# Performance work log

Hardware: AMD Instinct MI355X
Metric: run time of the kernel (lower is better)

Reference implementation:

```python
import jax, jax.numpy as jnp
import numpy as np

N, E, D, ED, H, MAXDEG = 50000, 800000, 128, 64, 8, 512
C = D // H


def _ln(x, g, b, eps=1e-5):
    m = jnp.mean(x, axis=-1, keepdims=True)
    v = jnp.var(x, axis=-1, keepdims=True)
    return (x - m) * jax.lax.rsqrt(v + eps) * g + b


def setup_inputs() -> dict:
    key = jax.random.key(0)
    ks = jax.random.split(key, 16)
    nrm = lambda k, s: jax.random.normal(k, s, jnp.float32) * 0.02
    return {
        "x": jax.random.normal(ks[0], (N, D), jnp.float32),
        "edge_index": jax.random.randint(ks[1], (2, E), 0, N, dtype=jnp.int32),
        "edge_attr": jax.random.normal(ks[2], (E, ED), jnp.float32),
        "deg_emb": nrm(ks[3], (MAXDEG, D)),
        "ln_g": jnp.ones((D,), jnp.float32), "ln_b": jnp.zeros((D,), jnp.float32),
        "Wq": nrm(ks[4], (D, D)), "bq": jnp.zeros((D,), jnp.float32),
        "Wk": nrm(ks[5], (D, D)), "bk": jnp.zeros((D,), jnp.float32),
        "Wv": nrm(ks[6], (D, D)), "bv": jnp.zeros((D,), jnp.float32),
        "We": nrm(ks[7], (ED, D)), "be": jnp.zeros((D,), jnp.float32),
        "Wskip": nrm(ks[8], (D, D)), "bskip": jnp.zeros((D,), jnp.float32),
        "W1": nrm(ks[9], (D, 4 * D)), "b1": jnp.zeros((4 * D,), jnp.float32),
        "W2": nrm(ks[10], (4 * D, D)), "b2": jnp.zeros((D,), jnp.float32),
        "eu_ln_g": jnp.ones((D,), jnp.float32), "eu_ln_b": jnp.zeros((D,), jnp.float32),
        "Wm": nrm(ks[11], (2 * D + ED, 2 * ED)), "bm": jnp.zeros((2 * ED,), jnp.float32),
        "eln_g": jnp.ones((ED,), jnp.float32), "eln_b": jnp.zeros((ED,), jnp.float32),
    }


def reference(x, edge_index, edge_attr, deg_emb, ln_g, ln_b, Wq, bq, Wk, bk, Wv, bv,
              We, be, Wskip, bskip, W1, b1, W2, b2, eu_ln_g, eu_ln_b, Wm, bm, eln_g, eln_b):
    n = x.shape[0]
    src, dst = edge_index[0], edge_index[1]

    # degree embedding: out-degree via scatter-add on src, clamped
    deg = jax.ops.segment_sum(jnp.ones_like(src), src, num_segments=n)
    x_in = x + deg_emb[jnp.clip(deg, 0, MAXDEG - 1)]

    # pre-norm (same LayerNorm module used for attn and ffn branches)
    h = _ln(x_in, ln_g, ln_b)

    # TransformerConv: per-edge gather -> score -> segment softmax -> scatter
    q = (h @ Wq + bq).reshape(n, H, C)
    k = (h @ Wk + bk).reshape(n, H, C)
    v = (h @ Wv + bv).reshape(n, H, C)
    e = (edge_attr @ We + be).reshape(-1, H, C)  # [E,H,C]

    ke = k[src] + e
    alpha = jnp.sum(q[dst] * ke, axis=-1) / jnp.sqrt(jnp.float32(C))  # [E,H]
    amax = jax.ops.segment_max(alpha, dst, num_segments=n)
    amax = jnp.where(jnp.isfinite(amax), amax, 0.0)
    ex = jnp.exp(alpha - amax[dst])
    denom = jax.ops.segment_sum(ex, dst, num_segments=n)
    w = ex / (denom[dst] + 1e-16)  # [E,H]

    msg = (v[src] + e) * w[:, :, None]
    out = jax.ops.segment_sum(msg, dst, num_segments=n).reshape(n, D)
    h_attn = out + h @ Wskip + bskip  # root skip on normed input

    x_attn = x_in + h_attn

    # FFN with pre-norm (norm_type == 'layer')
    hf = _ln(x_attn, ln_g, ln_b)
    ffn = jax.nn.gelu(hf @ W1 + b1, approximate=False) @ W2 + b2
    x_new = x_attn + ffn

    # EdgeUpdate: gated residual MLP on gathered node pairs
    xn = _ln(x_new, eu_ln_g, eu_ln_b)
    m = jnp.concatenate([xn[src], xn[dst], edge_attr], axis=-1)  # [E, 2D+ED]
    raw = jax.nn.relu(m @ Wm + bm)
    delta, gate = jnp.split(raw, 2, axis=-1)
    ea_new = _ln(edge_attr + jax.nn.sigmoid(gate) * delta, eln_g, eln_b)

    return x_new, ea_new
```

## Files before the change

### kernel.cpp

```cpp
#include <hip/hip_runtime.h>
#include <hip/hip_bf16.h>
#include <math.h>

constexpr int N_NODES = 50000;
constexpr int N_EDGES = 800000;
constexpr int D  = 128;
constexpr int ED = 64;

typedef __attribute__((ext_vector_type(8))) short short8;
typedef __attribute__((ext_vector_type(4))) float f32x4;

static __device__ __forceinline__ float allsum64(float v){
#pragma unroll
  for(int off=32; off>=1; off>>=1) v += __shfl_xor(v, off, 64);
  return v;
}

static __device__ __forceinline__ short bfs(float f){
  __hip_bfloat16 h = __float2bfloat16(f);
  return *reinterpret_cast<short*>(&h);
}
static __device__ __forceinline__ float bf2f(short s){
  __hip_bfloat16 h = *reinterpret_cast<__hip_bfloat16*>(&s);
  return __bfloat162float(h);
}
static __device__ __forceinline__ float lo16(int w){ return bf2f((short)(w & 0xffff)); }
static __device__ __forceinline__ float hi16(int w){ return bf2f((short)(((unsigned)w) >> 16)); }

template<typename T> __device__ __forceinline__ T cvt_out(float v);
template<> __device__ __forceinline__ float cvt_out<float>(float v){ return v; }
template<> __device__ __forceinline__ __hip_bfloat16 cvt_out<__hip_bfloat16>(float v){ return __float2bfloat16(v); }

__global__ void k_deg(const int* __restrict__ src, const int* __restrict__ dst,
                      int* __restrict__ deg, int* __restrict__ hist){
  int i = blockIdx.x*256 + threadIdx.x;
  if(i < N_EDGES){
    atomicAdd(&deg[src[i]], 1);
    atomicAdd(&hist[dst[i]], 1);
  }
}

__global__ __launch_bounds__(1024) void k_scan(const int* __restrict__ hist,
                                               int* __restrict__ rows,
                                               int* __restrict__ cursor){
  __shared__ int part[1024];
  const int t = threadIdx.x;
  const int CH = (N_NODES + 1023) / 1024;
  int base = t*CH;
  int s = 0;
  for(int i=0;i<CH;i++){ int idx=base+i; if(idx<N_NODES) s += hist[idx]; }
  part[t] = s; __syncthreads();
  for(int off=1; off<1024; off<<=1){
    int v = (t>=off) ? part[t-off] : 0;
    __syncthreads();
    part[t] += v;
    __syncthreads();
  }
  int run = part[t] - s;
  for(int i=0;i<CH;i++){
    int idx=base+i;
    if(idx<N_NODES){ rows[idx]=run; cursor[idx]=run; run += hist[idx]; }
  }
  if(t==1023) rows[N_NODES] = run;
}

__global__ void k_scatter(const int* __restrict__ src, const int* __restrict__ dst,
                          int* __restrict__ cursor,
                          int* __restrict__ perm, int* __restrict__ ssrc){
  int e = blockIdx.x*256 + threadIdx.x;
  if(e < N_EDGES){
    int p = atomicAdd(&cursor[dst[e]], 1);
    perm[p] = e;
    ssrc[p] = src[e];
  }
}

__global__ __launch_bounds__(256) void k_node_prep(
    const float* __restrict__ x, const int* __restrict__ deg,
    const float* __restrict__ deg_emb, const float* __restrict__ g,
    const float* __restrict__ b, float* __restrict__ xin, short* __restrict__ h){
  int node = blockIdx.x*4 + (threadIdx.x>>6);
  int lane = threadIdx.x & 63;
  if(node >= N_NODES) return;
  int dg = deg[node]; dg = dg > 511 ? 511 : dg;
  const float* xr = x + (size_t)node*D;
  const float* er = deg_emb + (size_t)dg*D;
  float a0 = xr[lane]    + er[lane];
  float a1 = xr[lane+64] + er[lane+64];
  float* xo = xin + (size_t)node*D;
  xo[lane] = a0; xo[lane+64] = a1;
  float s  = allsum64(a0+a1);
  float s2 = allsum64(a0*a0 + a1*a1);
  float mean = s * (1.f/128.f);
  float var  = s2 * (1.f/128.f) - mean*mean;
  float rs = rsqrtf(var + 1e-5f);
  h[(size_t)node*D + lane]    = bfs((a0-mean)*rs*g[lane]    + b[lane]);
  h[(size_t)node*D + lane+64] = bfs((a1-mean)*rs*g[lane+64] + b[lane+64]);
}

__global__ void k_pack(const float* __restrict__ Wq, const float* __restrict__ Wk,
                       const float* __restrict__ Wv, const float* __restrict__ Ws,
                       const float* __restrict__ bq, const float* __restrict__ bk,
                       const float* __restrict__ bv, const float* __restrict__ bs,
                       float* __restrict__ Wcat, float* __restrict__ bcat){
  int idx = blockIdx.x*256 + threadIdx.x;
  if(idx < D*4*D){
    int i = idx >> 9, j = idx & 511;
    int sel = j >> 7, jj = j & 127;
    const float* W = sel==0?Wq: sel==1?Wk: sel==2?Wv:Ws;
    Wcat[idx] = W[i*D + jj];
  } else if(idx < D*4*D + 4*D){
    int j = idx - D*4*D;
    int sel = j>>7, jj = j&127;
    const float* B = sel==0?bq: sel==1?bk: sel==2?bv:bs;
    bcat[j] = B[jj];
  }
}

__global__ void k_packWN(const float* __restrict__ W, short* __restrict__ out,
                         int K, int Nfull){
  int idx = blockIdx.x*256 + threadIdx.x;
  if(idx >= K*Nfull) return;
  int KC = K >> 5;
  int j  = idx & 7;
  int l  = (idx>>3) & 63;
  int cf = (idx>>9) & 7;
  int rest = idx >> 12;
  int kc = rest % KC;
  int nb = rest / KC;
  int k = kc*32 + ((l>>4)<<3) + j;
  int n = nb*128 + (cf<<4) + (l&15);
  out[idx] = bfs(W[(size_t)k*Nfull + n]);
}

__global__ void k_packWm12(const float* __restrict__ Wm, short* __restrict__ out){
  int idx = blockIdx.x*256 + threadIdx.x;
  if(idx >= 256*128) return;
  int j  = idx & 7;
  int l  = (idx>>3) & 63;
  int cf = (idx>>9) & 7;
  int rest = idx >> 12;
  int kc = rest & 3, nb = rest >> 2;
  int k = kc*32 + ((l>>4)<<3) + j;
  int n = (cf<<4) + (l&15);
  out[idx] = bfs(Wm[(size_t)(nb*128 + k)*128 + n]);
}

template<int ACT, int OMAP, typename OutT, typename AT>
__global__ __launch_bounds__(256) void k_gemm_mfma(
    const AT* __restrict__ A, const short* __restrict__ Wp,
    const float* __restrict__ bias,
    OutT* __restrict__ C, int M, int K, int Nfull){
  const int tid = threadIdx.x, lane = tid & 63, wid = tid >> 6;
  const int l16 = lane & 15, lg = lane >> 4;
  const int KC = K >> 5;
  const size_t rowb = (size_t)blockIdx.x*64 + wid*16;
  const int nb = blockIdx.y;
  size_t arow = rowb + l16; if(arow >= (size_t)M) arow = M-1;
  f32x4 acc[8] = {};
  const short8* Bg = ((const short8*)Wp) + (size_t)nb*KC*512 + lane;
  for(int kc=0; kc<KC; kc++){
    short8 a;
    if constexpr (sizeof(AT)==4){
      const float* ap = (const float*)A + arow*K + kc*32 + lg*8;
      float4 f0 = *(const float4*)ap;
      float4 f1 = *(const float4*)(ap+4);
      a[0]=bfs(f0.x); a[1]=bfs(f0.y); a[2]=bfs(f0.z); a[3]=bfs(f0.w);
      a[4]=bfs(f1.x); a[5]=bfs(f1.y); a[6]=bfs(f1.z); a[7]=bfs(f1.w);
    } else {
      a = *(const short8*)((const short*)A + arow*K + kc*32 + lg*8);
    }
#pragma unroll
    for(int cf=0;cf<8;cf++){
      short8 b = Bg[(kc*8+cf)*64];
      acc[cf] = __builtin_amdgcn_mfma_f32_16x16x32_bf16(a, b, acc[cf], 0, 0, 0);
    }
  }
#pragma unroll
  for(int cf=0;cf<8;cf++){
    int cIn = cf*16 + l16;
    int col = nb*128 + cIn;
    float bb = bias[col];
    int stCol;
    if(OMAP == 1){
      if(nb==0)      stCol = 2*(cIn&63) + (cIn>>6);
      else if(nb==1) stCol = 128 + 4*(cIn&63) + (cIn>>6);
      else if(nb==2) stCol = 128 + 4*(cIn&63) + 2 + (cIn>>6);
      else           stCol = 384 + 2*(cIn&63) + (cIn>>6);
    } else if(OMAP == 2){
      stCol = nb*128 + (cIn&15)*8 + (cIn>>4);
    } else stCol = col;
#pragma unroll
    for(int r=0;r<4;r++){
      size_t ro = rowb + lg*4 + r;
      if(ro < (size_t)M){
        float v = acc[cf][r] + bb;
        if(ACT == 1) v = v * 0.5f * (1.f + erff(v * 0.70710678118f));
        C[ro*Nfull + stCol] = cvt_out<OutT>(v);
      }
    }
  }
}

__global__ __launch_bounds__(256) void k_ffn2_ln(
    const short* __restrict__ A, const short* __restrict__ Wp,
    const float* __restrict__ bias, const float* __restrict__ Src,
    const float* __restrict__ g, const float* __restrict__ bv,
    float* __restrict__ xnew, short* __restrict__ xn, int M){
  const int tid = threadIdx.x, lane = tid & 63, wid = tid >> 6;
  const int l16 = lane & 15, lg = lane >> 4;
  const size_t rowb = (size_t)blockIdx.x*64 + wid*16;
  size_t arow = rowb + l16; if(arow >= (size_t)M) arow = M-1;
  f32x4 acc[8] = {};
  const short8* Bg = ((const short8*)Wp) + lane;
  for(int kc=0; kc<16; kc++){
    short8 a = *(const short8*)(A + arow*512 + kc*32 + lg*8);
#pragma unroll
    for(int cf=0;cf<8;cf++){
      short8 b = Bg[(kc*8+cf)*64];
      acc[cf] = __builtin_amdgcn_mfma_f32_16x16x32_bf16(a, b, acc[cf], 0, 0, 0);
    }
  }
  float vals[8][4];
#pragma unroll
  for(int cf=0;cf<8;cf++){
    int col = cf*16 + l16;
    float bb = bias[col];
#pragma unroll
    for(int r=0;r<4;r++){
      size_t ro = rowb + lg*4 + r; if(ro >= (size_t)M) ro = M-1;
      vals[cf][r] = acc[cf][r] + bb + Src[ro*128 + col];
    }
  }
#pragma unroll
  for(int r=0;r<4;r++){
    float s1 = 0.f, s2 = 0.f;
#pragma unroll
    for(int cf=0;cf<8;cf++){ s1 += vals[cf][r]; s2 += vals[cf][r]*vals[cf][r]; }
#pragma unroll
    for(int off=1; off<16; off<<=1){
      s1 += __shfl_xor(s1, off, 64);
      s2 += __shfl_xor(s2, off, 64);
    }
    float mean = s1 * (1.f/128.f);
    float var  = s2 * (1.f/128.f) - mean*mean;
    float rs = rsqrtf(var + 1e-5f);
    size_t ro = rowb + lg*4 + r;
    if(ro < (size_t)M){
#pragma unroll
      for(int cf=0;cf<8;cf++){
        int col = cf*16 + l16;
        xnew[ro*128 + col] = vals[cf][r];
        xn[ro*128 + col] = bfs((vals[cf][r]-mean)*rs*g[col] + bv[col]);
      }
    }
  }
}

__global__ __launch_bounds__(256) void k_eproj_sorted(
    const float* __restrict__ eattr, const int* __restrict__ perm,
    const short* __restrict__ Wep, const float* __restrict__ be,
    short* __restrict__ out){
  const int tid = threadIdx.x, lane = tid & 63, wid = tid >> 6;
  const int l16 = lane & 15, lg = lane >> 4;
  const size_t row = (size_t)blockIdx.x*64 + wid*16;
  const int pe = perm[row + l16];
  f32x4 acc[8] = {};
  const short8* Bg = ((const short8*)Wep) + lane;
  const float* ga = eattr + (size_t)pe*64;
#pragma unroll
  for(int kc=0;kc<2;kc++){
    int cb = kc*32 + lg*8;
    float4 f0 = *(const float4*)(ga + cb);
    float4 f1 = *(const float4*)(ga + cb + 4);
    short8 a;
    a[0]=bfs(f0.x); a[1]=bfs(f0.y); a[2]=bfs(f0.z); a[3]=bfs(f0.w);
    a[4]=bfs(f1.x); a[5]=bfs(f1.y); a[6]=bfs(f1.z); a[7]=bfs(f1.w);
#pragma unroll
    for(int cf=0;cf<8;cf++){
      short8 b = Bg[(kc*8+cf)*64];
      acc[cf] = __builtin_amdgcn_mfma_f32_16x16x32_bf16(a, b, acc[cf], 0, 0, 0);
    }
  }
#pragma unroll
  for(int cf=0;cf<8;cf++){
    int col = cf*16 + l16;
    int stCol = 2*(col&63) + (col>>6);
    float bb = be[col];
#pragma unroll
    for(int r=0;r<4;r++){
      size_t ro = row + lg*4 + r;
      out[ro*128 + stCol] = bfs(acc[cf][r] + bb);
    }
  }
}

__global__ __launch_bounds__(256) void k_attn_fused3(
    const int* __restrict__ ssrc, const int* __restrict__ rows,
    const short* __restrict__ qk, const short* __restrict__ es,
    const float* __restrict__ xin, const float* __restrict__ g,
    const float* __restrict__ b,
    float* __restrict__ xattn, short* __restrict__ hf){
  int n = blockIdx.x*4 + (threadIdx.x>>6);
  int lane = threadIdx.x & 63;
  if(n >= N_NODES) return;
  const short* qrow = qk + (size_t)n*512;
  int qw = *(const int*)(qrow + 2*lane);
  float q0 = lo16(qw), q1 = hi16(qw);
  float m0=-INFINITY, m1=-INFINITY;
  float den0=0.f, den1=0.f, acc0=0.f, acc1=0.f;
  int i = rows[n];
  const int i1 = rows[n+1];

  for(; i+2 <= i1; i += 2){
    int sA = ssrc[i], sB = ssrc[i+1];
    int ewA = *(const int*)(es + (size_t)i*128 + 2*lane);
    int ewB = *(const int*)(es + (size_t)(i+1)*128 + 2*lane);
    int2 kvA = *(const int2*)(qk + (size_t)sA*512 + 128 + 4*lane);
    int2 kvB = *(const int2*)(qk + (size_t)sB*512 + 128 + 4*lane);
    float eA0=lo16(ewA), eA1=hi16(ewA);
    float eB0=lo16(ewB), eB1=hi16(ewB);
    float pA0 = q0*(lo16(kvA.x)+eA0), pA1 = q1*(hi16(kvA.x)+eA1);
    float pB0 = q0*(lo16(kvB.x)+eB0), pB1 = q1*(hi16(kvB.x)+eB1);
#pragma unroll
    for(int off=1; off<16; off<<=1){
      pA0 += __shfl_xor(pA0,off,64); pA1 += __shfl_xor(pA1,off,64);
      pB0 += __shfl_xor(pB0,off,64); pB1 += __shfl_xor(pB1,off,64);
    }
    {
      float a0 = pA0*0.25f, a1 = pA1*0.25f;
      float v0 = lo16(kvA.y)+eA0, v1 = hi16(kvA.y)+eA1;
      float mn0 = fmaxf(m0,a0), mn1 = fmaxf(m1,a1);
      float sc0 = __expf(m0-mn0), sc1 = __expf(m1-mn1);
      float ex0 = __expf(a0-mn0), ex1 = __expf(a1-mn1);
      den0 = den0*sc0 + ex0;       den1 = den1*sc1 + ex1;
      acc0 = acc0*sc0 + ex0*v0;    acc1 = acc1*sc1 + ex1*v1;
      m0 = mn0; m1 = mn1;
    }
    {
      float a0 = pB0*0.25f, a1 = pB1*0.25f;
      float v0 = lo16(kvB.y)+eB0, v1 = hi16(kvB.y)+eB1;
      float mn0 = fmaxf(m0,a0), mn1 = fmaxf(m1,a1);
      float sc0 = __expf(m0-mn0), sc1 = __expf(m1-mn1);
      float ex0 = __expf(a0-mn0), ex1 = __expf(a1-mn1);
      den0 = den0*sc0 + ex0;       den1 = den1*sc1 + ex1;
      acc0 = acc0*sc0 + ex0*v0;    acc1 = acc1*sc1 + ex1*v1;
      m0 = mn0; m1 = mn1;
    }
  }
  if(i < i1){
    int sA = ssrc[i];
    int ewA = *(const int*)(es + (size_t)i*128 + 2*lane);
    int2 kvA = *(const int2*)(qk + (size_t)sA*512 + 128 + 4*lane);
    float eA0=lo16(ewA), eA1=hi16(ewA);
    float pA0 = q0*(lo16(kvA.x)+eA0), pA1 = q1*(hi16(kvA.x)+eA1);
#pragma unroll
    for(int off=1; off<16; off<<=1){
      pA0 += __shfl_xor(pA0,off,64); pA1 += __shfl_xor(pA1,off,64);
    }
    float a0 = pA0*0.25f, a1 = pA1*0.25f;
    float v0 = lo16(kvA.y)+eA0, v1 = hi16(kvA.y)+eA1;
    float mn0 = fmaxf(m0,a0), mn1 = fmaxf(m1,a1);
    float sc0 = __expf(m0-mn0), sc1 = __expf(m1-mn1);
    float ex0 = __expf(a0-mn0), ex1 = __expf(a1-mn1);
    den0 = den0*sc0 + ex0;       den1 = den1*sc1 + ex1;
    acc0 = acc0*sc0 + ex0*v0;    acc1 = acc1*sc1 + ex1*v1;
    m0 = mn0; m1 = mn1;
  }

  float o0 = acc0/(den0+1e-16f);
  float o1 = acc1/(den1+1e-16f);
  int sw = *(const int*)(qrow + 384 + 2*lane);
  size_t base = (size_t)n*128;
  float a0 = xin[base+lane]    + o0 + lo16(sw);
  float a1 = xin[base+lane+64] + o1 + hi16(sw);
  xattn[base+lane] = a0; xattn[base+lane+64] = a1;
  float s  = allsum64(a0+a1);
  float s2 = allsum64(a0*a0 + a1*a1);
  float mean = s * (1.f/128.f);
  float var  = s2 * (1.f/128.f) - mean*mean;
  float rs = rsqrtf(var + 1e-5f);
  hf[base+lane]    = bfs((a0-mean)*rs*g[lane]    + b[lane]);
  hf[base+lane+64] = bfs((a1-mean)*rs*g[lane+64] + b[lane+64]);
}

__global__ __launch_bounds__(256) void k_edge_mfma6(
    const int* __restrict__ src, const int* __restrict__ dst,
    const short* __restrict__ P12, const float* __restrict__ ea,
    const short* __restrict__ Wmep, const float* __restrict__ bm,
    const float* __restrict__ eg, const float* __restrict__ ebv,
    float* __restrict__ out){
  const int tid = threadIdx.x, lane = tid & 63, wid = tid >> 6;
  const int l16 = lane & 15, lg = lane >> 4;
  const size_t e0 = (size_t)blockIdx.x*128 + wid*32;
  const int ko = lg*8;
  f32x4 acc[8][2] = {};
  const short8* Bg = ((const short8*)Wmep) + lane;

#pragma unroll
  for(int kc=0; kc<2; kc++){
    short8 a[2];
#pragma unroll
    for(int mi=0;mi<2;mi++){
      const float* ap = ea + (e0 + mi*16 + l16)*64 + kc*32 + ko;
      float4 f0 = *(const float4*)ap;
      float4 f1 = *(const float4*)(ap+4);
      a[mi][0]=bfs(f0.x); a[mi][1]=bfs(f0.y); a[mi][2]=bfs(f0.z); a[mi][3]=bfs(f0.w);
      a[mi][4]=bfs(f1.x); a[mi][5]=bfs(f1.y); a[mi][6]=bfs(f1.z); a[mi][7]=bfs(f1.w);
    }
#pragma unroll
    for(int cf=0;cf<8;cf++){
      short8 b = Bg[(kc*8+cf)*64];
      acc[cf][0] = __builtin_amdgcn_mfma_f32_16x16x32_bf16(a[0], b, acc[cf][0], 0, 0, 0);
      acc[cf][1] = __builtin_amdgcn_mfma_f32_16x16x32_bf16(a[1], b, acc[cf][1], 0, 0, 0);
    }
  }

#pragma unroll
  for(int mi=0;mi<2;mi++){
#pragma unroll
    for(int r=0;r<4;r++){
      size_t erow = e0 + mi*16 + lg*4 + r;
      int sE = src[erow], dE = dst[erow];
      short8 p1 = *(const short8*)(P12 + (size_t)sE*256 + l16*8);
      short8 p2 = *(const short8*)(P12 + (size_t)dE*256 + 128 + l16*8);
#pragma unroll
      for(int cf=0;cf<8;cf++)
        acc[cf][mi][r] += bf2f(p1[cf]) + bf2f(p2[cf]);
    }
  }

  float bmd[4], bmg[4], egc[4], ebc[4];
#pragma unroll
  for(int cf=0;cf<4;cf++){
    int col = cf*16 + l16;
    bmd[cf] = bm[col];
    bmg[cf] = bm[64+col];
    egc[cf] = eg[col];
    ebc[cf] = ebv[col];
  }
#pragma unroll
  for(int mi=0;mi<2;mi++){
#pragma unroll
    for(int r=0;r<4;r++){
      size_t erow = e0 + mi*16 + lg*4 + r;
      float u[4];
      float s1 = 0.f, s2 = 0.f;
#pragma unroll
      for(int cf=0;cf<4;cf++){
        float dlt = fmaxf(0.f, acc[cf][mi][r]   + bmd[cf]);
        float gt  = fmaxf(0.f, acc[cf+4][mi][r] + bmg[cf]);
        float uu = ea[erow*64 + cf*16 + l16] + dlt / (1.f + expf(-gt));
        u[cf] = uu; s1 += uu; s2 += uu*uu;
      }
#pragma unroll
      for(int off=1; off<16; off<<=1){
        s1 += __shfl_xor(s1, off, 64);
        s2 += __shfl_xor(s2, off, 64);
      }
      float mean = s1 * (1.f/64.f);
      float var  = s2 * (1.f/64.f) - mean*mean;
      float rs = rsqrtf(var + 1e-5f);
#pragma unroll
      for(int cf=0;cf<4;cf++)
        out[erow*64 + cf*16 + l16] = (u[cf]-mean)*rs*egc[cf] + ebc[cf];
    }
  }
}

extern "C" void kernel_launch(void* const* d_in, const int* in_sizes, int n_in,
                              void* d_out, int out_size, void* d_ws, size_t ws_size,
                              hipStream_t stream){
  const float* x       = (const float*)d_in[0];
  const int*   eidx    = (const int*)d_in[1];
  const float* eattr   = (const float*)d_in[2];
  const float* deg_emb = (const float*)d_in[3];
  const float* ln_g = (const float*)d_in[4];
  const float* ln_b = (const float*)d_in[5];
  const float* Wq = (const float*)d_in[6];  const float* bq = (const float*)d_in[7];
  const float* Wk = (const float*)d_in[8];  const float* bk = (const float*)d_in[9];
  const float* Wv = (const float*)d_in[10]; const float* bv = (const float*)d_in[11];
  const float* We = (const float*)d_in[12]; const float* be = (const float*)d_in[13];
  const float* Ws = (const float*)d_in[14]; const float* bs = (const float*)d_in[15];
  const float* W1 = (const float*)d_in[16]; const float* b1 = (const float*)d_in[17];
  const float* W2 = (const float*)d_in[18]; const float* b2 = (const float*)d_in[19];
  const float* eug = (const float*)d_in[20]; const float* eub = (const float*)d_in[21];
  const float* Wm = (const float*)d_in[22]; const float* bm = (const float*)d_in[23];
  const float* eg = (const float*)d_in[24]; const float* eb = (const float*)d_in[25];
  (void)in_sizes; (void)n_in; (void)out_size; (void)ws_size;

  const int* src = eidx;
  const int* dst = eidx + N_EDGES;

  float* ws = (float*)d_ws;
  size_t o = 0;
  auto alloc = [&](size_t n){ size_t r = o; o += (n + 63) & ~(size_t)63; return r; };
  size_t o_deg   = alloc(N_NODES);
  size_t o_hist  = alloc(N_NODES);
  size_t o_zb    = alloc(256);
  size_t zero_f  = o;
  size_t o_rows  = alloc(N_NODES+1);
  size_t o_cur   = alloc(N_NODES);
  size_t o_perm  = alloc(N_EDGES);
  size_t o_ssrc  = alloc(N_EDGES);
  size_t o_attn  = alloc((size_t)N_NODES*D);
  size_t o_xin   = alloc((size_t)N_NODES*D);
  size_t o_h     = alloc((size_t)N_NODES*D/2);
  size_t o_qkv16 = alloc((size_t)N_NODES*256);
  size_t o_p12   = alloc((size_t)N_NODES*128);
  size_t o_wcat  = alloc((size_t)D*4*D);
  size_t o_bcat  = alloc(4*D);
  size_t o_wqp   = alloc((size_t)128*512/2);
  size_t o_w1p   = alloc((size_t)128*512/2);
  size_t o_w2p   = alloc((size_t)512*128/2);
  size_t o_wm12  = alloc((size_t)256*128/2);
  size_t o_wmep  = alloc((size_t)64*128/2);
  size_t o_wep   = alloc((size_t)64*128/2);

  float* xnew_out = (float*)d_out;
  float* ea_out   = xnew_out + (size_t)N_NODES*D;
  short* es = (short*)ea_out;

  hipMemsetAsync(d_ws, 0, zero_f*sizeof(float), stream);

  k_deg<<<(N_EDGES+255)/256, 256, 0, stream>>>(src, dst, (int*)(ws+o_deg),
                                               (int*)(ws+o_hist));
  k_scan<<<1, 1024, 0, stream>>>((int*)(ws+o_hist), (int*)(ws+o_rows),
                                 (int*)(ws+o_cur));
  k_scatter<<<(N_EDGES+255)/256, 256, 0, stream>>>(src, dst, (int*)(ws+o_cur),
                                                   (int*)(ws+o_perm),
                                                   (int*)(ws+o_ssrc));
  k_node_prep<<<N_NODES/4, 256, 0, stream>>>(x, (int*)(ws+o_deg), deg_emb, ln_g, ln_b,
                                             ws+o_xin, (short*)(ws+o_h));
  k_pack<<<(D*4*D + 4*D + 255)/256, 256, 0, stream>>>(Wq,Wk,Wv,Ws, bq,bk,bv,bs,
                                                      ws+o_wcat, ws+o_bcat);
  k_packWN<<<256, 256, 0, stream>>>(ws+o_wcat, (short*)(ws+o_wqp), 128, 512);
  k_packWN<<<256, 256, 0, stream>>>(W1, (short*)(ws+o_w1p), 128, 512);
  k_packWN<<<256, 256, 0, stream>>>(W2, (short*)(ws+o_w2p), 512, 128);
  k_packWm12<<<128, 256, 0, stream>>>(Wm, (short*)(ws+o_wm12));
  k_packWN<<<32,  256, 0, stream>>>(Wm + 256*128, (short*)(ws+o_wmep), 64, 128);
  k_packWN<<<32,  256, 0, stream>>>(We, (short*)(ws+o_wep), 64, 128);
  {
    dim3 g((N_NODES+63)/64, 4);
    k_gemm_mfma<0,1,__hip_bfloat16,short><<<g,256,0,stream>>>(
        (const short*)(ws+o_h), (const short*)(ws+o_wqp), ws+o_bcat,
        (__hip_bfloat16*)(ws+o_qkv16), N_NODES, 128, 512);
  }
  k_eproj_sorted<<<N_EDGES/64, 256, 0, stream>>>(eattr, (const int*)(ws+o_perm),
                                                 (const short*)(ws+o_wep), be, es);
  k_attn_fused3<<<(N_NODES+3)/4, 256, 0, stream>>>((const int*)(ws+o_ssrc),
                                                   (int*)(ws+o_rows),
                                                   (const short*)(ws+o_qkv16), es,
                                                   ws+o_xin, ln_g, ln_b,
                                                   ws+o_attn, (short*)(ws+o_h));
  {
    dim3 g((N_NODES+63)/64, 4);
    k_gemm_mfma<1,0,__hip_bfloat16,short><<<g,256,0,stream>>>(
        (const short*)(ws+o_h), (const short*)(ws+o_w1p), b1,
        (__hip_bfloat16*)(ws+o_qkv16), N_NODES, 128, 512);
  }
  {
    dim3 g((N_NODES+63)/64);
    k_ffn2_ln<<<g,256,0,stream>>>(
        (const short*)(ws+o_qkv16), (const short*)(ws+o_w2p), b2, ws+o_attn,
        eug, eub, xnew_out, (short*)(ws+o_xin), N_NODES);
  }
  {
    dim3 g((N_NODES+63)/64, 2);
    k_gemm_mfma<0,2,__hip_bfloat16,short><<<g,256,0,stream>>>(
        (const short*)(ws+o_xin), (const short*)(ws+o_wm12), ws+o_zb,
        (__hip_bfloat16*)(ws+o_p12), N_NODES, 128, 256);
  }
  k_edge_mfma6<<<N_EDGES/128, 256, 0, stream>>>(src, dst, (const short*)(ws+o_p12),
                                                eattr, (const short*)(ws+o_wmep), bm,
                                                eg, eb, ea_out);
}
```

Baseline: 859.9 us.

## Fuse edge projection into attention kernel and fold edge bias into node GEMM

The separate edge-projection kernel, which wrote bf16 per-edge projections to global memory, is removed. The attention kernel now computes the projection for each chunk of 16 incoming edges with MFMA and keeps the result in shared memory. The edge-MLP bias moves into the per-node P12 GEMM through a packed bias buffer, and the edge kernel's sigmoid switches to fast exp plus a hardware reciprocal. This cuts an 800K-edge round trip through global memory, in exchange for partially wasted MFMA work on low-degree nodes and extra LDS use per block.

```diff
diff --git a/kernel.cpp b/kernel.cpp
--- a/kernel.cpp
+++ b/kernel.cpp
@@ -26,6 +26,9 @@
 }
 static __device__ __forceinline__ float lo16(int w){ return bf2f((short)(w & 0xffff)); }
 static __device__ __forceinline__ float hi16(int w){ return bf2f((short)(((unsigned)w) >> 16)); }
+static __device__ __forceinline__ int pack2(float lo, float hi){
+  return (int)((unsigned short)bfs(lo)) | ((int)bfs(hi) << 16);
+}
 
 template<typename T> __device__ __forceinline__ T cvt_out(float v);
 template<> __device__ __forceinline__ float cvt_out<float>(float v){ return v; }
@@ -115,6 +118,11 @@
     const float* B = sel==0?bq: sel==1?bk: sel==2?bv:bs;
     bcat[j] = B[jj];
   }
+}
+
+__global__ void k_bmcat(const float* __restrict__ bm, float* __restrict__ out){
+  int i = threadIdx.x;
+  out[i] = (i < 128) ? bm[i] : 0.f;
 }
 
 __global__ void k_packWN(const float* __restrict__ W, short* __restrict__ out,
@@ -257,77 +265,106 @@
   }
 }
 
-__global__ __launch_bounds__(256) void k_eproj_sorted(
-    const float* __restrict__ eattr, const int* __restrict__ perm,
-    const short* __restrict__ Wep, const float* __restrict__ be,
-    short* __restrict__ out){
-  const int tid = threadIdx.x, lane = tid & 63, wid = tid >> 6;
+__global__ __launch_bounds__(256) void k_attn_fused5(
+    const int* __restrict__ ssrc, const int* __restrict__ rows,
+    const int* __restrict__ perm,
+    const float* __restrict__ eattr, const short* __restrict__ Wep,
+    const float* __restrict__ be,
+    const short* __restrict__ qk, const float* __restrict__ xin,
+    const float* __restrict__ g, const float* __restrict__ b,
+    float* __restrict__ xattn, short* __restrict__ hf){
+  __shared__ int esb[4][16*64];
+  const int w = threadIdx.x >> 6;
+  const int lane = threadIdx.x & 63;
+  const int n = blockIdx.x*4 + w;
+  if(n >= N_NODES) return;
   const int l16 = lane & 15, lg = lane >> 4;
-  const size_t row = (size_t)blockIdx.x*64 + wid*16;
-  const int pe = perm[row + l16];
-  f32x4 acc[8] = {};
-  const short8* Bg = ((const short8*)Wep) + lane;
-  const float* ga = eattr + (size_t)pe*64;
-#pragma unroll
-  for(int kc=0;kc<2;kc++){
-    int cb = kc*32 + lg*8;
-    float4 f0 = *(const float4*)(ga + cb);
-    float4 f1 = *(const float4*)(ga + cb + 4);
-    short8 a;
-    a[0]=bfs(f0.x); a[1]=bfs(f0.y); a[2]=bfs(f0.z); a[3]=bfs(f0.w);
-    a[4]=bfs(f1.x); a[5]=bfs(f1.y); a[6]=bfs(f1.z); a[7]=bfs(f1.w);
-#pragma unroll
-    for(int cf=0;cf<8;cf++){
-      short8 b = Bg[(kc*8+cf)*64];
-      acc[cf] = __builtin_amdgcn_mfma_f32_16x16x32_bf16(a, b, acc[cf], 0, 0, 0);
-    }
-  }
-#pragma unroll
-  for(int cf=0;cf<8;cf++){
-    int col = cf*16 + l16;
-    int stCol = 2*(col&63) + (col>>6);
-    float bb = be[col];
-#pragma unroll
-    for(int r=0;r<4;r++){
-      size_t ro = row + lg*4 + r;
-      out[ro*128 + stCol] = bfs(acc[cf][r] + bb);
-    }
-  }
-}
-
-__global__ __launch_bounds__(256) void k_attn_fused3(
-    const int* __restrict__ ssrc, const int* __restrict__ rows,
-    const short* __restrict__ qk, const short* __restrict__ es,
-    const float* __restrict__ xin, const float* __restrict__ g,
-    const float* __restrict__ b,
-    float* __restrict__ xattn, short* __restrict__ hf){
-  int n = blockIdx.x*4 + (threadIdx.x>>6);
-  int lane = threadIdx.x & 63;
-  if(n >= N_NODES) return;
   const short* qrow = qk + (size_t)n*512;
   int qw = *(const int*)(qrow + 2*lane);
   float q0 = lo16(qw), q1 = hi16(qw);
   float m0=-INFINITY, m1=-INFINITY;
   float den0=0.f, den1=0.f, acc0=0.f, acc1=0.f;
-  int i = rows[n];
-  const int i1 = rows[n+1];
-
-  for(; i+2 <= i1; i += 2){
-    int sA = ssrc[i], sB = ssrc[i+1];
-    int ewA = *(const int*)(es + (size_t)i*128 + 2*lane);
-    int ewB = *(const int*)(es + (size_t)(i+1)*128 + 2*lane);
-    int2 kvA = *(const int2*)(qk + (size_t)sA*512 + 128 + 4*lane);
-    int2 kvB = *(const int2*)(qk + (size_t)sB*512 + 128 + 4*lane);
-    float eA0=lo16(ewA), eA1=hi16(ewA);
-    float eB0=lo16(ewB), eB1=hi16(ewB);
-    float pA0 = q0*(lo16(kvA.x)+eA0), pA1 = q1*(hi16(kvA.x)+eA1);
-    float pB0 = q0*(lo16(kvB.x)+eB0), pB1 = q1*(hi16(kvB.x)+eB1);
-#pragma unroll
-    for(int off=1; off<16; off<<=1){
-      pA0 += __shfl_xor(pA0,off,64); pA1 += __shfl_xor(pA1,off,64);
-      pB0 += __shfl_xor(pB0,off,64); pB1 += __shfl_xor(pB1,off,64);
-    }
+  const int i0 = rows[n], i1 = rows[n+1];
+  const short8* Bg = ((const short8*)Wep) + lane;
+  int* myes = esb[w];
+
+  for(int i = i0; i < i1; i += 16){
+    int cnt = i1 - i; if(cnt > 16) cnt = 16;
     {
+      int ridx = i + l16; if(ridx >= i1) ridx = i1 - 1;
+      int pe = perm[ridx];
+      const float* ga = eattr + (size_t)pe*64;
+      f32x4 eacc[8] = {};
+#pragma unroll
+      for(int kc=0;kc<2;kc++){
+        const float* ap = ga + kc*32 + lg*8;
+        float4 f0 = *(const float4*)ap;
+        float4 f1 = *(const float4*)(ap+4);
+        short8 a;
+        a[0]=bfs(f0.x); a[1]=bfs(f0.y); a[2]=bfs(f0.z); a[3]=bfs(f0.w);
+        a[4]=bfs(f1.x); a[5]=bfs(f1.y); a[6]=bfs(f1.z); a[7]=bfs(f1.w);
+#pragma unroll
+        for(int cf=0;cf<8;cf++){
+          short8 bfrag = Bg[(kc*8+cf)*64];
+          eacc[cf] = __builtin_amdgcn_mfma_f32_16x16x32_bf16(a, bfrag, eacc[cf], 0, 0, 0);
+        }
+      }
+#pragma unroll
+      for(int cf=0;cf<4;cf++){
+        int col = cf*16 + l16;
+        float blo = be[col], bhi = be[col+64];
+#pragma unroll
+        for(int r=0;r<4;r++)
+          myes[(lg*4+r)*64 + col] = pack2(eacc[cf][r] + blo, eacc[cf+4][r] + bhi);
+      }
+    }
+    int j = 0;
+    for(; j+2 <= cnt; j += 2){
+      int sA = ssrc[i+j], sB = ssrc[i+j+1];
+      int ewA = myes[(j  )*64 + lane];
+      int ewB = myes[(j+1)*64 + lane];
+      int2 kvA = *(const int2*)(qk + (size_t)sA*512 + 128 + 4*lane);
+      int2 kvB = *(const int2*)(qk + (size_t)sB*512 + 128 + 4*lane);
+      float eA0=lo16(ewA), eA1=hi16(ewA);
+      float eB0=lo16(ewB), eB1=hi16(ewB);
+      float pA0 = q0*(lo16(kvA.x)+eA0), pA1 = q1*(hi16(kvA.x)+eA1);
+      float pB0 = q0*(lo16(kvB.x)+eB0), pB1 = q1*(hi16(kvB.x)+eB1);
+#pragma unroll
+      for(int off=1; off<16; off<<=1){
+        pA0 += __shfl_xor(pA0,off,64); pA1 += __shfl_xor(pA1,off,64);
+        pB0 += __shfl_xor(pB0,off,64); pB1 += __shfl_xor(pB1,off,64);
+      }
+      {
+        float a0 = pA0*0.25f, a1 = pA1*0.25f;
+        float v0 = lo16(kvA.y)+eA0, v1 = hi16(kvA.y)+eA1;
+        float mn0 = fmaxf(m0,a0), mn1 = fmaxf(m1,a1);
+        float sc0 = __expf(m0-mn0), sc1 = __expf(m1-mn1);
+        float ex0 = __expf(a0-mn0), ex1 = __expf(a1-mn1);
+        den0 = den0*sc0 + ex0;       den1 = den1*sc1 + ex1;
+        acc0 = acc0*sc0 + ex0*v0;    acc1 = acc1*sc1 + ex1*v1;
+        m0 = mn0; m1 = mn1;
+      }
+      {
+        float a0 = pB0*0.25f, a1 = pB1*0.25f;
+        float v0 = lo16(kvB.y)+eB0, v1 = hi16(kvB.y)+eB1;
+        float mn0 = fmaxf(m0,a0), mn1 = fmaxf(m1,a1);
+        float sc0 = __expf(m0-mn0), sc1 = __expf(m1-mn1);
+        float ex0 = __expf(a0-mn0), ex1 = __expf(a1-mn1);
+        den0 = den0*sc0 + ex0;       den1 = den1*sc1 + ex1;
+        acc0 = acc0*sc0 + ex0*v0;    acc1 = acc1*sc1 + ex1*v1;
+        m0 = mn0; m1 = mn1;
+      }
+    }
+    if(j < cnt){
+      int sA = ssrc[i+j];
+      int ewA = myes[j*64 + lane];
+      int2 kvA = *(const int2*)(qk + (size_t)sA*512 + 128 + 4*lane);
+      float eA0=lo16(ewA), eA1=hi16(ewA);
+      float pA0 = q0*(lo16(kvA.x)+eA0), pA1 = q1*(hi16(kvA.x)+eA1);
+#pragma unroll
+      for(int off=1; off<16; off<<=1){
+        pA0 += __shfl_xor(pA0,off,64); pA1 += __shfl_xor(pA1,off,64);
+      }
       float a0 = pA0*0.25f, a1 = pA1*0.25f;
       float v0 = lo16(kvA.y)+eA0, v1 = hi16(kvA.y)+eA1;
       float mn0 = fmaxf(m0,a0), mn1 = fmaxf(m1,a1);
@@ -337,35 +374,6 @@
       acc0 = acc0*sc0 + ex0*v0;    acc1 = acc1*sc1 + ex1*v1;
       m0 = mn0; m1 = mn1;
     }
-    {
-      float a0 = pB0*0.25f, a1 = pB1*0.25f;
-      float v0 = lo16(kvB.y)+eB0, v1 = hi16(kvB.y)+eB1;
-      float mn0 = fmaxf(m0,a0), mn1 = fmaxf(m1,a1);
-      float sc0 = __expf(m0-mn0), sc1 = __expf(m1-mn1);
-      float ex0 = __expf(a0-mn0), ex1 = __expf(a1-mn1);
-      den0 = den0*sc0 + ex0;       den1 = den1*sc1 + ex1;
-      acc0 = acc0*sc0 + ex0*v0;    acc1 = acc1*sc1 + ex1*v1;
-      m0 = mn0; m1 = mn1;
-    }
-  }
-  if(i < i1){
-    int sA = ssrc[i];
-    int ewA = *(const int*)(es + (size_t)i*128 + 2*lane);
-    int2 kvA = *(const int2*)(qk + (size_t)sA*512 + 128 + 4*lane);
-    float eA0=lo16(ewA), eA1=hi16(ewA);
-    float pA0 = q0*(lo16(kvA.x)+eA0), pA1 = q1*(hi16(kvA.x)+eA1);
-#pragma unroll
-    for(int off=1; off<16; off<<=1){
-      pA0 += __shfl_xor(pA0,off,64); pA1 += __shfl_xor(pA1,off,64);
-    }
-    float a0 = pA0*0.25f, a1 = pA1*0.25f;
-    float v0 = lo16(kvA.y)+eA0, v1 = hi16(kvA.y)+eA1;
-    float mn0 = fmaxf(m0,a0), mn1 = fmaxf(m1,a1);
-    float sc0 = __expf(m0-mn0), sc1 = __expf(m1-mn1);
-    float ex0 = __expf(a0-mn0), ex1 = __expf(a1-mn1);
-    den0 = den0*sc0 + ex0;       den1 = den1*sc1 + ex1;
-    acc0 = acc0*sc0 + ex0*v0;    acc1 = acc1*sc1 + ex1*v1;
-    m0 = mn0; m1 = mn1;
   }
 
   float o0 = acc0/(den0+1e-16f);
@@ -384,10 +392,10 @@
   hf[base+lane+64] = bfs((a1-mean)*rs*g[lane+64] + b[lane+64]);
 }
 
-__global__ __launch_bounds__(256) void k_edge_mfma6(
+__global__ __launch_bounds__(256) void k_edge_mfma7(
     const int* __restrict__ src, const int* __restrict__ dst,
     const short* __restrict__ P12, const float* __restrict__ ea,
-    const short* __restrict__ Wmep, const float* __restrict__ bm,
+    const short* __restrict__ Wmep,
     const float* __restrict__ eg, const float* __restrict__ ebv,
     float* __restrict__ out){
   const int tid = threadIdx.x, lane = tid & 63, wid = tid >> 6;
@@ -430,12 +438,10 @@
     }
   }
 
-  float bmd[4], bmg[4], egc[4], ebc[4];
+  float egc[4], ebc[4];
 #pragma unroll
   for(int cf=0;cf<4;cf++){
     int col = cf*16 + l16;
-    bmd[cf] = bm[col];
-    bmg[cf] = bm[64+col];
     egc[cf] = eg[col];
     ebc[cf] = ebv[col];
   }
@@ -448,9 +454,10 @@
       float s1 = 0.f, s2 = 0.f;
 #pragma unroll
       for(int cf=0;cf<4;cf++){
-        float dlt = fmaxf(0.f, acc[cf][mi][r]   + bmd[cf]);
-        float gt  = fmaxf(0.f, acc[cf+4][mi][r] + bmg[cf]);
-        float uu = ea[erow*64 + cf*16 + l16] + dlt / (1.f + expf(-gt));
+        float dlt = fmaxf(0.f, acc[cf][mi][r]);
+        float gt  = fmaxf(0.f, acc[cf+4][mi][r]);
+        float sig = __builtin_amdgcn_rcpf(1.f + __expf(-gt));
+        float uu = ea[erow*64 + cf*16 + l16] + dlt * sig;
         u[cf] = uu; s1 += uu; s2 += uu*uu;
       }
 #pragma unroll
@@ -497,7 +504,6 @@
   auto alloc = [&](size_t n){ size_t r = o; o += (n + 63) & ~(size_t)63; return r; };
   size_t o_deg   = alloc(N_NODES);
   size_t o_hist  = alloc(N_NODES);
-  size_t o_zb    = alloc(256);
   size_t zero_f  = o;
   size_t o_rows  = alloc(N_NODES+1);
   size_t o_cur   = alloc(N_NODES);
@@ -510,6 +516,7 @@
   size_t o_p12   = alloc((size_t)N_NODES*128);
   size_t o_wcat  = alloc((size_t)D*4*D);
   size_t o_bcat  = alloc(4*D);
+  size_t o_bmcat = alloc(256);
   size_t o_wqp   = alloc((size_t)128*512/2);
   size_t o_w1p   = alloc((size_t)128*512/2);
   size_t o_w2p   = alloc((size_t)512*128/2);
@@ -519,7 +526,6 @@
 
   float* xnew_out = (float*)d_out;
   float* ea_out   = xnew_out + (size_t)N_NODES*D;
-  short* es = (short*)ea_out;
 
   hipMemsetAsync(d_ws, 0, zero_f*sizeof(float), stream);
 
@@ -534,6 +540,7 @@
                                              ws+o_xin, (short*)(ws+o_h));
   k_pack<<<(D*4*D + 4*D + 255)/256, 256, 0, stream>>>(Wq,Wk,Wv,Ws, bq,bk,bv,bs,
                                                       ws+o_wcat, ws+o_bcat);
+  k_bmcat<<<1, 256, 0, stream>>>(bm, ws+o_bmcat);
   k_packWN<<<256, 256, 0, stream>>>(ws+o_wcat, (short*)(ws+o_wqp), 128, 512);
   k_packWN<<<256, 256, 0, stream>>>(W1, (short*)(ws+o_w1p), 128, 512);
   k_packWN<<<256, 256, 0, stream>>>(W2, (short*)(ws+o_w2p), 512, 128);
@@ -546,13 +553,11 @@
         (const short*)(ws+o_h), (const short*)(ws+o_wqp), ws+o_bcat,
         (__hip_bfloat16*)(ws+o_qkv16), N_NODES, 128, 512);
   }
-  k_eproj_sorted<<<N_EDGES/64, 256, 0, stream>>>(eattr, (const int*)(ws+o_perm),
-                                                 (const short*)(ws+o_wep), be, es);
-  k_attn_fused3<<<(N_NODES+3)/4, 256, 0, stream>>>((const int*)(ws+o_ssrc),
-                                                   (int*)(ws+o_rows),
-                                                   (const short*)(ws+o_qkv16), es,
-                                                   ws+o_xin, ln_g, ln_b,
-                                                   ws+o_attn, (short*)(ws+o_h));
+  k_attn_fused5<<<(N_NODES+3)/4, 256, 0, stream>>>(
+      (const int*)(ws+o_ssrc), (int*)(ws+o_rows), (const int*)(ws+o_perm),
+      eattr, (const short*)(ws+o_wep), be,
+      (const short*)(ws+o_qkv16), ws+o_xin, ln_g, ln_b,
+      ws+o_attn, (short*)(ws+o_h));
   {
     dim3 g((N_NODES+63)/64, 4);
     k_gemm_mfma<1,0,__hip_bfloat16,short><<<g,256,0,stream>>>(
@@ -568,10 +573,10 @@
   {
     dim3 g((N_NODES+63)/64, 2);
     k_gemm_mfma<0,2,__hip_bfloat16,short><<<g,256,0,stream>>>(
-        (const short*)(ws+o_xin), (const short*)(ws+o_wm12), ws+o_zb,
+        (const short*)(ws+o_xin), (const short*)(ws+o_wm12), ws+o_bmcat,
         (__hip_bfloat16*)(ws+o_p12), N_NODES, 128, 256);
   }
-  k_edge_mfma6<<<N_EDGES/128, 256, 0, stream>>>(src, dst, (const short*)(ws+o_p12),
-                                                eattr, (const short*)(ws+o_wmep), bm,
+  k_edge_mfma7<<<N_EDGES/128, 256, 0, stream>>>(src, dst, (const short*)(ws+o_p12),
+                                                eattr, (const short*)(ws+o_wmep),
                                                 eg, eb, ea_out);
 }
```

Result: slower. 1.039 ms (+20.8%).
